# Kernel optimization log

Hardware: AMD Instinct MI355X
Metric: run time of the kernel (lower is better)

Reference implementation:

```python
import jax, jax.numpy as jnp
import numpy as np

EPS = 1e-5  # torch BatchNorm1d default

def _bn(z, g, b):
    # training-mode BatchNorm1d: per-feature batch mean, biased variance
    m = jnp.mean(z, axis=0)
    v = jnp.mean((z - m) ** 2, axis=0)
    return (z - m) * jax.lax.rsqrt(v + EPS) * g + b

def _cell(x, h, c, Wx, Wh, gx, bx, gh, bh):
    gates = _bn(x @ Wx.T, gx, bx) + _bn(h @ Wh.T, gh, bh)  # [B, 4H]
    f, i, o, g = jnp.split(gates, 4, axis=1)  # chunk order f,i,o,g
    c2 = jax.nn.sigmoid(f) * c + jax.nn.sigmoid(i) * jnp.tanh(g)
    h2 = jax.nn.sigmoid(o) * jnp.tanh(c2)
    return h2, c2

def setup_inputs() -> dict:
    key = jax.random.key(0)
    B, H, OUT = 16384, 512, 256
    IN0 = 257  # input_size - 1 (x_dim 256 + y_dim 1)
    ks = jax.random.split(key, 16)
    def lin(k, fo, fi):
        s = 1.0 / np.sqrt(fi)
        return jax.random.uniform(k, (fo, fi), jnp.float32, -s, s)
    return {
        "x": jax.random.normal(ks[0], (B, 256), jnp.float32),
        "y": jax.random.normal(ks[1], (B, 1), jnp.float32),
        "h0": jax.random.normal(ks[2], (2, B, H), jnp.float32),
        "c0": jax.random.normal(ks[3], (2, B, H), jnp.float32),
        "Wx0": lin(ks[4], 4 * H, IN0),
        "Wh0": lin(ks[5], 4 * H, H),
        "gx0": jnp.ones((4 * H,), jnp.float32),
        "bx0": jnp.zeros((4 * H,), jnp.float32),
        "gh0": jnp.ones((4 * H,), jnp.float32),
        "bh0": jnp.zeros((4 * H,), jnp.float32),
        "Wx1": lin(ks[6], 4 * H, H),
        "Wh1": lin(ks[7], 4 * H, H),
        "gx1": jnp.ones((4 * H,), jnp.float32),
        "bx1": jnp.zeros((4 * H,), jnp.float32),
        "gh1": jnp.ones((4 * H,), jnp.float32),
        "bh1": jnp.zeros((4 * H,), jnp.float32),
        "Wo": lin(ks[8], OUT, H),
        "bo": jnp.zeros((OUT,), jnp.float32),
    }

def reference(x, y, h0, c0, Wx0, Wh0, gx0, bx0, gh0, bh0,
              Wx1, Wh1, gx1, bx1, gh1, bh1, Wo, bo):
    inp = jnp.concatenate([x, y], axis=1)  # [B, 257]
    h1, c1 = _cell(inp, h0[0], c0[0], Wx0, Wh0, gx0, bx0, gh0, bh0)
    h2, c2 = _cell(h1, h0[1], c0[1], Wx1, Wh1, gx1, bx1, gh1, bh1)
    out = h2 @ Wo.T + bo  # [B, output_size]
    return (out, jnp.stack([h1, h2]), jnp.stack([c1, c2]))
```

## Files before the change

### kernel.cpp

```cpp
#include <hip/hip_runtime.h>
#include <cstdint>

typedef unsigned short u16;
typedef unsigned int u32;
typedef float floatx4 __attribute__((ext_vector_type(4)));
typedef __bf16 bf16x8 __attribute__((ext_vector_type(8)));
typedef u16 u16x4 __attribute__((ext_vector_type(4)));

__device__ __forceinline__ u16 f2b(float f) {
  u32 u = __builtin_bit_cast(u32, f);
  u32 r = (u + 0x7fffu + ((u >> 16) & 1u)) >> 16;
  return (u16)r;
}
__device__ __forceinline__ float b2f(u16 b) {
  return __builtin_bit_cast(float, (u32)b << 16);
}
__device__ __forceinline__ float sigf(float x) { return 1.f / (1.f + __expf(-x)); }
__device__ __forceinline__ float tanhfast(float x) { return 2.f / (1.f + __expf(-2.f * x)) - 1.f; }

#define GLDS(gp, lp) __builtin_amdgcn_global_load_lds( \
    (const __attribute__((address_space(1))) u32*)(gp), \
    (__attribute__((address_space(3))) u32*)(lp), 16, 0, 0)

template <int STATS, int BIAS>
__global__ __launch_bounds__(256) void gemm_bt(
    const u16* __restrict__ A, const u16* __restrict__ W, void* __restrict__ Cv,
    int N, int K, float* __restrict__ ssum, float* __restrict__ ssq,
    const float* __restrict__ bias) {
  __shared__ u16 As[128 * 32];
  __shared__ u16 Bs[128 * 32];
  const int tid = threadIdx.x;
  const int lane = tid & 63;
  const int wave = tid >> 6;
  const int wm = (wave >> 1) << 6;
  const int wn = (wave & 1) << 6;
  const int m0 = blockIdx.y * 128;
  const int n0 = blockIdx.x * 128;
  const u16* Ab = A + (size_t)m0 * K;
  const u16* Wb = W + (size_t)n0 * K;
  const size_t soff = (size_t)(tid >> 2) * K + ((tid & 3) << 3);
  const size_t soff2 = soff + (size_t)64 * K;
  const int fr = lane & 15;
  const int fq = lane >> 4;
  const int aoff = fr * 32 + fq * 8;

  floatx4 acc[4][4] = {};

  for (int k0 = 0; k0 < K; k0 += 32) {
    __syncthreads();
    GLDS(Ab + soff + k0, &As[tid * 8]);
    GLDS(Ab + soff2 + k0, &As[tid * 8 + 2048]);
    GLDS(Wb + soff + k0, &Bs[tid * 8]);
    GLDS(Wb + soff2 + k0, &Bs[tid * 8 + 2048]);
    __syncthreads();
    bf16x8 af[4], bfv[4];
#pragma unroll
    for (int i = 0; i < 4; ++i) af[i] = *(const bf16x8*)&As[(wm + i * 16) * 32 + aoff];
#pragma unroll
    for (int j = 0; j < 4; ++j) bfv[j] = *(const bf16x8*)&Bs[(wn + j * 16) * 32 + aoff];
#pragma unroll
    for (int i = 0; i < 4; ++i)
#pragma unroll
      for (int j = 0; j < 4; ++j)
        acc[i][j] = __builtin_amdgcn_mfma_f32_16x16x32_bf16(af[i], bfv[j], acc[i][j], 0, 0, 0);
  }

  if (BIAS) {
    float* C = (float*)Cv;
#pragma unroll
    for (int i = 0; i < 4; ++i)
#pragma unroll
      for (int j = 0; j < 4; ++j) {
        const int col = n0 + wn + j * 16 + fr;
        const float bv = bias[col];
#pragma unroll
        for (int r = 0; r < 4; ++r) {
          const int row = m0 + wm + i * 16 + fq * 4 + r;
          C[(size_t)row * N + col] = acc[i][j][r] + bv;
        }
      }
  } else {
    u16* C = (u16*)Cv;
#pragma unroll
    for (int i = 0; i < 4; ++i)
#pragma unroll
      for (int j = 0; j < 4; ++j) {
        const int col = n0 + wn + j * 16 + fr;
#pragma unroll
        for (int r = 0; r < 4; ++r) {
          const int row = m0 + wm + i * 16 + fq * 4 + r;
          C[(size_t)row * N + col] = f2b(acc[i][j][r]);
        }
      }
  }

  if (STATS) {
#pragma unroll
    for (int j = 0; j < 4; ++j) {
      float s = 0.f, q = 0.f;
#pragma unroll
      for (int i = 0; i < 4; ++i)
#pragma unroll
        for (int r = 0; r < 4; ++r) {
          const float v = acc[i][j][r];
          s += v;
          q += v * v;
        }
      s += __shfl_xor(s, 16);
      s += __shfl_xor(s, 32);
      q += __shfl_xor(q, 16);
      q += __shfl_xor(q, 32);
      if (fq == 0) {
        atomicAdd(&ssum[n0 + wn + j * 16 + fr], s);
        atomicAdd(&ssq[n0 + wn + j * 16 + fr], q);
      }
    }
  }
}

__global__ void pad_inp_k(const float* __restrict__ x, const float* __restrict__ y,
                          u16* __restrict__ o) {
  const int idx = blockIdx.x * 256 + threadIdx.x;
  const int b = idx / 288;
  const int c = idx - b * 288;
  float v = 0.f;
  if (c < 256) v = x[b * 256 + c];
  else if (c == 256) v = y[b];
  o[idx] = f2b(v);
}

__global__ void pad_w_k(const float* __restrict__ w, u16* __restrict__ o) {
  const int idx = blockIdx.x * 256 + threadIdx.x;
  const int r = idx / 288;
  const int c = idx - r * 288;
  o[idx] = f2b(c < 257 ? w[r * 257 + c] : 0.f);
}

__global__ void f2b_k(const float4* __restrict__ in, u16x4* __restrict__ o, int n4) {
  const int idx = blockIdx.x * 256 + threadIdx.x;
  if (idx < n4) {
    const float4 v = in[idx];
    u16x4 r;
    r.x = f2b(v.x);
    r.y = f2b(v.y);
    r.z = f2b(v.z);
    r.w = f2b(v.w);
    o[idx] = r;
  }
}

__global__ void coef_k(const float* __restrict__ st, const float* __restrict__ gx,
                       const float* __restrict__ bx, const float* __restrict__ gh,
                       const float* __restrict__ bh, float* __restrict__ cf, float invB) {
  const int j = blockIdx.x * 256 + threadIdx.x;
  const float mx = st[j] * invB;
  const float vx = st[2048 + j] * invB - mx * mx;
  const float ax = gx[j] * rsqrtf(vx + 1e-5f);
  const float mh = st[4096 + j] * invB;
  const float vh = st[6144 + j] * invB - mh * mh;
  const float ah = gh[j] * rsqrtf(vh + 1e-5f);
  cf[j] = ax;
  cf[2048 + j] = ah;
  cf[4096 + j] = bx[j] - mx * ax + bh[j] - mh * ah;
}

__global__ void cell_k(const u16* __restrict__ Zx, const u16* __restrict__ Zh,
                       const float* __restrict__ coef, const float* __restrict__ cin,
                       float* __restrict__ hout, float* __restrict__ cout,
                       u16* __restrict__ hb) {
  const int idx = blockIdx.x * 256 + threadIdx.x;
  const int b = idx >> 8;
  const int j2 = (idx & 255) << 1;
  const size_t rb = (size_t)b << 11;
  float gv[4][2];
#pragma unroll
  for (int g = 0; g < 4; ++g) {
    const int col = (g << 9) + j2;
    const u32 zx = *(const u32*)(Zx + rb + col);
    const u32 zh = *(const u32*)(Zh + rb + col);
#pragma unroll
    for (int t = 0; t < 2; ++t) {
      const float zxv = b2f((u16)(zx >> (16 * t)));
      const float zhv = b2f((u16)(zh >> (16 * t)));
      gv[g][t] = coef[col + t] * zxv + coef[2048 + col + t] * zhv + coef[4096 + col + t];
    }
  }
  const size_t ob = ((size_t)b << 9) + j2;
  const float2 cp = *(const float2*)(cin + ob);
  float cn[2], hn[2];
#pragma unroll
  for (int t = 0; t < 2; ++t) {
    const float cprev = t ? cp.y : cp.x;
    const float cc = sigf(gv[0][t]) * cprev + sigf(gv[1][t]) * tanhfast(gv[3][t]);
    cn[t] = cc;
    hn[t] = sigf(gv[2][t]) * tanhfast(cc);
  }
  *(float2*)(cout + ob) = make_float2(cn[0], cn[1]);
  *(float2*)(hout + ob) = make_float2(hn[0], hn[1]);
  *(u32*)(hb + ob) = (u32)f2b(hn[0]) | ((u32)f2b(hn[1]) << 16);
}

extern "C" void kernel_launch(void* const* d_in, const int* in_sizes, int n_in,
                              void* d_out, int out_size, void* d_ws, size_t ws_size,
                              hipStream_t stream) {
  (void)in_sizes; (void)n_in; (void)out_size; (void)ws_size;
  constexpr int B = 16384, H = 512, G = 2048, KP = 288, K1 = 512, NOUT = 256;

  const float* x = (const float*)d_in[0];
  const float* y = (const float*)d_in[1];
  const float* h0 = (const float*)d_in[2];
  const float* c0 = (const float*)d_in[3];
  const float* Wx0 = (const float*)d_in[4];
  const float* Wh0 = (const float*)d_in[5];
  const float* gx0 = (const float*)d_in[6];
  const float* bx0 = (const float*)d_in[7];
  const float* gh0 = (const float*)d_in[8];
  const float* bh0 = (const float*)d_in[9];
  const float* Wx1 = (const float*)d_in[10];
  const float* Wh1 = (const float*)d_in[11];
  const float* gx1 = (const float*)d_in[12];
  const float* bx1 = (const float*)d_in[13];
  const float* gh1 = (const float*)d_in[14];
  const float* bh1 = (const float*)d_in[15];
  const float* Wo = (const float*)d_in[16];
  const float* bo = (const float*)d_in[17];

  char* p = (char*)d_ws;
  u16* Zx = (u16*)p;   p += (size_t)B * G * 2;
  u16* Zh = (u16*)p;   p += (size_t)B * G * 2;
  u16* h0b = (u16*)p;  p += (size_t)2 * B * H * 2;
  u16* h1b = (u16*)p;  p += (size_t)B * H * 2;
  u16* inpb = (u16*)p; p += (size_t)B * KP * 2;
  u16* wx0b = (u16*)p; p += (size_t)G * KP * 2;
  u16* wh0b = (u16*)p; p += (size_t)G * K1 * 2;
  u16* wx1b = (u16*)p; p += (size_t)G * K1 * 2;
  u16* wh1b = (u16*)p; p += (size_t)G * K1 * 2;
  u16* wob = (u16*)p;  p += (size_t)NOUT * K1 * 2;
  float* stats = (float*)p; p += (size_t)8 * G * 4;
  float* coef = (float*)p;  p += (size_t)6 * G * 4;

  float* out_o = (float*)d_out;
  float* h_o = out_o + (size_t)B * NOUT;
  float* c_o = h_o + (size_t)2 * B * H;

  hipMemsetAsync(stats, 0, (size_t)8 * G * sizeof(float), stream);

  pad_inp_k<<<B * KP / 256, 256, 0, stream>>>(x, y, inpb);
  pad_w_k<<<G * KP / 256, 256, 0, stream>>>(Wx0, wx0b);
  f2b_k<<<2 * B * H / 4 / 256, 256, 0, stream>>>((const float4*)h0, (u16x4*)h0b, 2 * B * H / 4);
  f2b_k<<<G * K1 / 4 / 256, 256, 0, stream>>>((const float4*)Wh0, (u16x4*)wh0b, G * K1 / 4);
  f2b_k<<<G * K1 / 4 / 256, 256, 0, stream>>>((const float4*)Wx1, (u16x4*)wx1b, G * K1 / 4);
  f2b_k<<<G * K1 / 4 / 256, 256, 0, stream>>>((const float4*)Wh1, (u16x4*)wh1b, G * K1 / 4);
  f2b_k<<<NOUT * K1 / 4 / 256, 256, 0, stream>>>((const float4*)Wo, (u16x4*)wob, NOUT * K1 / 4);

  const dim3 blk(256);
  const dim3 gbig(G / 128, B / 128);

  gemm_bt<1, 0><<<gbig, blk, 0, stream>>>(inpb, wx0b, Zx, G, KP, stats + 0 * G, stats + 1 * G, nullptr);
  gemm_bt<1, 0><<<gbig, blk, 0, stream>>>(h0b, wh0b, Zh, G, K1, stats + 2 * G, stats + 3 * G, nullptr);
  coef_k<<<G / 256, 256, 0, stream>>>(stats, gx0, bx0, gh0, bh0, coef, 1.f / B);
  cell_k<<<B, 256, 0, stream>>>(Zx, Zh, coef, c0, h_o, c_o, h1b);

  gemm_bt<1, 0><<<gbig, blk, 0, stream>>>(h1b, wx1b, Zx, G, K1, stats + 4 * G, stats + 5 * G, nullptr);
  gemm_bt<1, 0><<<gbig, blk, 0, stream>>>(h0b + (size_t)B * H, wh1b, Zh, G, K1, stats + 6 * G, stats + 7 * G, nullptr);
  coef_k<<<G / 256, 256, 0, stream>>>(stats + 4 * G, gx1, bx1, gh1, bh1, coef + 3 * G, 1.f / B);
  cell_k<<<B, 256, 0, stream>>>(Zx, Zh, coef + 3 * G, c0 + (size_t)B * H,
                                h_o + (size_t)B * H, c_o + (size_t)B * H, h1b);

  const dim3 gout(NOUT / 128, B / 128);
  gemm_bt<0, 1><<<gout, blk, 0, stream>>>(h1b, wob, out_o, NOUT, K1, nullptr, nullptr, bo);
}
```

Before: 638.8 us.

## Replace gate GEMMs with 256x256-tile, 4-stage pipelined, swizzled-LDS kernel

```diff
diff --git a/kernel.cpp b/kernel.cpp
--- a/kernel.cpp
+++ b/kernel.cpp
@@ -21,6 +21,129 @@
 #define GLDS(gp, lp) __builtin_amdgcn_global_load_lds( \
     (const __attribute__((address_space(1))) u32*)(gp), \
     (__attribute__((address_space(3))) u32*)(lp), 16, 0, 0)
+
+template <int KT>
+__global__ __launch_bounds__(512, 2) void gemm256(
+    const u16* __restrict__ A, const u16* __restrict__ W, u16* __restrict__ C,
+    int N, float* __restrict__ ssum, float* __restrict__ ssq) {
+  constexpr int NT = KT / 32;
+  __shared__ __align__(16) u16 lds[4 * 16384];
+
+  const int tid = threadIdx.x;
+  const int lane = tid & 63;
+  const int wid = tid >> 6;
+  const int wm = (wid >> 2) << 7;
+  const int wn = (wid & 3) << 6;
+  const int fr = lane & 15;
+  const int fq = lane >> 4;
+
+  const int l = blockIdx.x + (blockIdx.y << 3);
+  const int xcd = l & 7;
+  const int idx = l >> 3;
+  const int bx = idx & 7;
+  const int by = (xcd << 3) + (idx >> 3);
+  const int m0 = by << 8;
+  const int n0 = bx << 8;
+
+  const u16* Ab = A + (size_t)m0 * KT;
+  const u16* Wb = W + (size_t)n0 * KT;
+
+  const int q0 = tid, q1 = tid + 512;
+  const int r0 = q0 >> 2, r1 = q1 >> 2;
+  const int c0 = (q0 & 3) ^ ((r0 >> 1) & 3);
+  const int c1 = (q1 & 3) ^ ((r1 >> 1) & 3);
+  const u16* pa0 = Ab + (size_t)r0 * KT + c0 * 8;
+  const u16* pa1 = Ab + (size_t)r1 * KT + c1 * 8;
+  const u16* pb0 = Wb + (size_t)r0 * KT + c0 * 8;
+  const u16* pb1 = Wb + (size_t)r1 * KT + c1 * 8;
+  const int d0 = q0 * 8;
+  const int d1 = q1 * 8;
+
+#define STAGE(kt) do {                                      \
+    const int _sl = ((kt) & 3) * 16384;                     \
+    const int _ko = (kt) * 32;                              \
+    GLDS(pa0 + _ko, &lds[_sl + d0]);                        \
+    GLDS(pa1 + _ko, &lds[_sl + d1]);                        \
+    GLDS(pb0 + _ko, &lds[_sl + 8192 + d0]);                 \
+    GLDS(pb1 + _ko, &lds[_sl + 8192 + d1]);                 \
+  } while (0)
+
+  int aoffs[8], boffs[4];
+#pragma unroll
+  for (int mf = 0; mf < 8; ++mf) {
+    const int R = wm + mf * 16 + fr;
+    aoffs[mf] = R * 32 + ((fq ^ ((R >> 1) & 3)) << 3);
+  }
+#pragma unroll
+  for (int nf = 0; nf < 4; ++nf) {
+    const int R = wn + nf * 16 + fr;
+    boffs[nf] = 8192 + R * 32 + ((fq ^ ((R >> 1) & 3)) << 3);
+  }
+
+  floatx4 acc[8][4] = {};
+
+  STAGE(0);
+  STAGE(1);
+  STAGE(2);
+
+#pragma unroll
+  for (int t = 0; t < NT; ++t) {
+    if (NT - 1 - t >= 2)      asm volatile("s_waitcnt vmcnt(8)" ::: "memory");
+    else if (NT - 1 - t == 1) asm volatile("s_waitcnt vmcnt(4)" ::: "memory");
+    else                      asm volatile("s_waitcnt vmcnt(0)" ::: "memory");
+    __builtin_amdgcn_s_barrier();
+    __builtin_amdgcn_sched_barrier(0);
+
+    if (t + 3 < NT) STAGE(t + 3);
+
+    const int sl = (t & 3) * 16384;
+    bf16x8 bfv[4];
+#pragma unroll
+    for (int nf = 0; nf < 4; ++nf) bfv[nf] = *(const bf16x8*)&lds[sl + boffs[nf]];
+#pragma unroll
+    for (int mf = 0; mf < 8; ++mf) {
+      const bf16x8 af = *(const bf16x8*)&lds[sl + aoffs[mf]];
+#pragma unroll
+      for (int nf = 0; nf < 4; ++nf)
+        acc[mf][nf] = __builtin_amdgcn_mfma_f32_16x16x32_bf16(af, bfv[nf], acc[mf][nf], 0, 0, 0);
+    }
+    asm volatile("s_waitcnt lgkmcnt(0)" ::: "memory");
+    __builtin_amdgcn_sched_barrier(0);
+  }
+#undef STAGE
+
+#pragma unroll
+  for (int mf = 0; mf < 8; ++mf)
+#pragma unroll
+    for (int nf = 0; nf < 4; ++nf) {
+      const int col = n0 + wn + nf * 16 + fr;
+#pragma unroll
+      for (int r = 0; r < 4; ++r) {
+        const int row = m0 + wm + mf * 16 + fq * 4 + r;
+        C[(size_t)row * N + col] = f2b(acc[mf][nf][r]);
+      }
+    }
+#pragma unroll
+  for (int nf = 0; nf < 4; ++nf) {
+    float s = 0.f, qv = 0.f;
+#pragma unroll
+    for (int mf = 0; mf < 8; ++mf)
+#pragma unroll
+      for (int r = 0; r < 4; ++r) {
+        const float v = acc[mf][nf][r];
+        s += v;
+        qv += v * v;
+      }
+    s += __shfl_xor(s, 16);
+    s += __shfl_xor(s, 32);
+    qv += __shfl_xor(qv, 16);
+    qv += __shfl_xor(qv, 32);
+    if (fq == 0) {
+      atomicAdd(&ssum[n0 + wn + nf * 16 + fr], s);
+      atomicAdd(&ssq[n0 + wn + nf * 16 + fr], qv);
+    }
+  }
+}
 
 template <int STATS, int BIAS>
 __global__ __launch_bounds__(256) void gemm_bt(
@@ -66,7 +189,7 @@
   }
 
   if (BIAS) {
-    float* C = (float*)Cv;
+    float* Cf = (float*)Cv;
 #pragma unroll
     for (int i = 0; i < 4; ++i)
 #pragma unroll
@@ -76,11 +199,11 @@
 #pragma unroll
         for (int r = 0; r < 4; ++r) {
           const int row = m0 + wm + i * 16 + fq * 4 + r;
-          C[(size_t)row * N + col] = acc[i][j][r] + bv;
+          Cf[(size_t)row * N + col] = acc[i][j][r] + bv;
         }
       }
   } else {
-    u16* C = (u16*)Cv;
+    u16* Cb = (u16*)Cv;
 #pragma unroll
     for (int i = 0; i < 4; ++i)
 #pragma unroll
@@ -89,7 +212,7 @@
 #pragma unroll
         for (int r = 0; r < 4; ++r) {
           const int row = m0 + wm + i * 16 + fq * 4 + r;
-          C[(size_t)row * N + col] = f2b(acc[i][j][r]);
+          Cb[(size_t)row * N + col] = f2b(acc[i][j][r]);
         }
       }
   }
@@ -253,20 +376,21 @@
   f2b_k<<<G * K1 / 4 / 256, 256, 0, stream>>>((const float4*)Wh1, (u16x4*)wh1b, G * K1 / 4);
   f2b_k<<<NOUT * K1 / 4 / 256, 256, 0, stream>>>((const float4*)Wo, (u16x4*)wob, NOUT * K1 / 4);
 
-  const dim3 blk(256);
-  const dim3 gbig(G / 128, B / 128);
-
-  gemm_bt<1, 0><<<gbig, blk, 0, stream>>>(inpb, wx0b, Zx, G, KP, stats + 0 * G, stats + 1 * G, nullptr);
-  gemm_bt<1, 0><<<gbig, blk, 0, stream>>>(h0b, wh0b, Zh, G, K1, stats + 2 * G, stats + 3 * G, nullptr);
+  const dim3 blk512(512);
+  const dim3 g256(G / 256, B / 256);
+
+  gemm256<KP><<<g256, blk512, 0, stream>>>(inpb, wx0b, Zx, G, stats + 0 * G, stats + 1 * G);
+  gemm256<K1><<<g256, blk512, 0, stream>>>(h0b, wh0b, Zh, G, stats + 2 * G, stats + 3 * G);
   coef_k<<<G / 256, 256, 0, stream>>>(stats, gx0, bx0, gh0, bh0, coef, 1.f / B);
   cell_k<<<B, 256, 0, stream>>>(Zx, Zh, coef, c0, h_o, c_o, h1b);
 
-  gemm_bt<1, 0><<<gbig, blk, 0, stream>>>(h1b, wx1b, Zx, G, K1, stats + 4 * G, stats + 5 * G, nullptr);
-  gemm_bt<1, 0><<<gbig, blk, 0, stream>>>(h0b + (size_t)B * H, wh1b, Zh, G, K1, stats + 6 * G, stats + 7 * G, nullptr);
+  gemm256<K1><<<g256, blk512, 0, stream>>>(h1b, wx1b, Zx, G, stats + 4 * G, stats + 5 * G);
+  gemm256<K1><<<g256, blk512, 0, stream>>>(h0b + (size_t)B * H, wh1b, Zh, G, stats + 6 * G, stats + 7 * G);
   coef_k<<<G / 256, 256, 0, stream>>>(stats + 4 * G, gx1, bx1, gh1, bh1, coef + 3 * G, 1.f / B);
   cell_k<<<B, 256, 0, stream>>>(Zx, Zh, coef + 3 * G, c0 + (size_t)B * H,
                                 h_o + (size_t)B * H, c_o + (size_t)B * H, h1b);
 
+  const dim3 blk(256);
   const dim3 gout(NOUT / 128, B / 128);
   gemm_bt<0, 1><<<gout, blk, 0, stream>>>(h1b, wob, out_o, NOUT, K1, nullptr, nullptr, bo);
 }
```

Result: faster. 612.1 us (-4.2%).
